# Kernel tuning notes

Measured on AMD Instinct MI355X. Metric: run time of the kernel, lower is better.

## Reference

```python
import jax, jax.numpy as jnp
import numpy as np
from jax import lax

B, T, IN, H, OUT = 4096, 512, 2, 12, 2


def setup_inputs() -> dict:
    key = jax.random.key(0)
    ks = jax.random.split(key, 11)
    s = 1.0 / np.sqrt(H)  # PyTorch LSTM init scale
    f32 = jnp.float32
    return {
        "x": jax.random.normal(ks[0], (B, T, IN), dtype=f32),
        "W_ih0": jax.random.uniform(ks[1], (4 * H, IN), dtype=f32, minval=-s, maxval=s),
        "W_hh0": jax.random.uniform(ks[2], (4 * H, H), dtype=f32, minval=-s, maxval=s),
        "b_ih0": jax.random.uniform(ks[3], (4 * H,), dtype=f32, minval=-s, maxval=s),
        "b_hh0": jax.random.uniform(ks[4], (4 * H,), dtype=f32, minval=-s, maxval=s),
        "W_ih1": jax.random.uniform(ks[5], (4 * H, H), dtype=f32, minval=-s, maxval=s),
        "W_hh1": jax.random.uniform(ks[6], (4 * H, H), dtype=f32, minval=-s, maxval=s),
        "b_ih1": jax.random.uniform(ks[7], (4 * H,), dtype=f32, minval=-s, maxval=s),
        "b_hh1": jax.random.uniform(ks[8], (4 * H,), dtype=f32, minval=-s, maxval=s),
        "fc_W": jax.random.uniform(ks[9], (OUT, H), dtype=f32, minval=-s, maxval=s),
        "fc_b": jax.random.uniform(ks[10], (OUT,), dtype=f32, minval=-s, maxval=s),
    }


def _lstm_layer(x, W_ih, W_hh, b_ih, b_hh):
    # x: [B, T, in_dim] -> hidden trajectory [B, T, H]
    b, h = x.shape[0], W_hh.shape[1]
    # Precompute input contribution for all timesteps: [T, B, 4H]
    xg = jnp.einsum('bti,gi->tbg', x, W_ih) + b_ih + b_hh

    def step(carry, xg_t):
        hprev, cprev = carry
        gates = xg_t + hprev @ W_hh.T  # [B, 4H], PyTorch gate order i,f,g,o
        i, f, g, o = jnp.split(gates, 4, axis=-1)
        i = jax.nn.sigmoid(i)
        f = jax.nn.sigmoid(f)
        g = jnp.tanh(g)
        o = jax.nn.sigmoid(o)
        c = f * cprev + i * g
        hnew = o * jnp.tanh(c)
        return (hnew, c), hnew

    z = jnp.zeros((b, h), dtype=x.dtype)
    _, hs = lax.scan(step, (z, z), xg)  # hs: [T, B, H]
    return jnp.swapaxes(hs, 0, 1)  # [B, T, H]


def reference(x, W_ih0, W_hh0, b_ih0, b_hh0, W_ih1, W_hh1, b_ih1, b_hh1, fc_W, fc_b):
    # 2-layer LSTM, h0=c0=0; dropout is identity in eval mode.
    h1 = _lstm_layer(x, W_ih0, W_hh0, b_ih0, b_hh0)   # [B, T, H]
    h2 = _lstm_layer(h1, W_ih1, W_hh1, b_ih1, b_hh1)  # [B, T, H]
    last = h2[:, -1, :]                               # [B, H]
    return last @ fc_W.T + fc_b                       # [B, OUT]
```

## Files before the change

### kernel.cpp

```cpp
#include <hip/hip_runtime.h>


namespace {
constexpr int H  = 12;
constexpr int T  = 512;
constexpr float LOG2E = 1.4426950408889634f;

typedef float f2 __attribute__((ext_vector_type(2)));
typedef float f4 __attribute__((ext_vector_type(4)));

__device__ __forceinline__ f2 pkfma(f2 a, f2 b, f2 c) {
    asm("v_pk_fma_f32 %0, %1, %2, %0" : "+v"(c) : "v"(a), "v"(b));
    return c;
}
__device__ __forceinline__ f2 pkmul(f2 a, f2 b) {
    f2 d; asm("v_pk_mul_f32 %0, %1, %2" : "=v"(d) : "v"(a), "v"(b)); return d;
}
__device__ __forceinline__ f2 pkadd(f2 a, f2 b) {
    f2 d; asm("v_pk_add_f32 %0, %1, %2" : "=v"(d) : "v"(a), "v"(b)); return d;
}
__device__ __forceinline__ float exp2_(float x) {
    float r; asm("v_exp_f32 %0, %1" : "=v"(r) : "v"(x)); return r;
}
__device__ __forceinline__ float rcp_(float x) { return __builtin_amdgcn_rcpf(x); }
__device__ __forceinline__ void memfence_() { asm volatile("" ::: "memory"); }

template <int CTRL>
__device__ __forceinline__ float dppf(float v) {
    return __int_as_float(__builtin_amdgcn_update_dpp(
        __float_as_int(v), __float_as_int(v), CTRL, 0xF, 0xF, true));
}
constexpr int QP1 = 0x39;
constexpr int QP2 = 0x4E;
constexpr int QP3 = 0x93;
}

__global__ __launch_bounds__(256, 4) void lstm2_fc_kernel(
    const float* __restrict__ x,
    const float* __restrict__ W_ih0,
    const float* __restrict__ W_hh0,
    const float* __restrict__ b_ih0,
    const float* __restrict__ b_hh0,
    const float* __restrict__ W_ih1,
    const float* __restrict__ W_hh1,
    const float* __restrict__ b_ih1,
    const float* __restrict__ b_hh1,
    const float* __restrict__ fc_W,
    const float* __restrict__ fc_b,
    float* __restrict__ out)
{
    const int lane = threadIdx.x & 63;
    const int wid  = __builtin_amdgcn_readfirstlane((int)threadIdx.x >> 6);
    const int b    = blockIdx.x * 4 + wid;
    const int u    = lane >> 2;
    const int gate = lane & 3;
    const int uc   = (u < H) ? u : 0;
    const int r    = gate * H + uc;

    const float pre  = (gate == 2) ? 2.0f : 1.0f;
    const float kmul = -LOG2E * pre;
    const float pa   = 1.0f - pre;
    const float km2  = -2.0f * LOG2E;

    __shared__ __align__(16) float sm[4 * 32];
    float* smb = &sm[wid * 32];
    const bool writer = (gate == 0) && (u < H);
    float* smw0 = smb + uc;
    float* smw1 = smb + 16 + uc;

    f2 wx, whh0p[6], wih1p[6], whh1p[6];
    wx.x = kmul * W_ih0[r * 2 + 0];
    wx.y = kmul * W_ih0[r * 2 + 1];
#pragma unroll
    for (int k = 0; k < 6; ++k) {
        whh0p[k].x = kmul * W_hh0[r * H + 2 * k];
        whh0p[k].y = kmul * W_hh0[r * H + 2 * k + 1];
        wih1p[k].x = kmul * W_ih1[r * H + 2 * k];
        wih1p[k].y = kmul * W_ih1[r * H + 2 * k + 1];
        whh1p[k].x = kmul * W_hh1[r * H + 2 * k];
        whh1p[k].y = kmul * W_hh1[r * H + 2 * k + 1];
    }
    f2 bias0p, bias1p;
    bias0p.x = kmul * (b_ih0[r] + b_hh0[r]); bias0p.y = 0.0f;
    bias1p.x = kmul * (b_ih1[r] + b_hh1[r]); bias1p.y = 0.0f;

    float c0 = 0.0f, c1 = 0.0f;
    f2 hp0[6], hq1[6];
#pragma unroll
    for (int k = 0; k < 6; ++k) { hp0[k] = (f2)(0.0f); hq1[k] = (f2)(0.0f); }

    const f4* xb4 = (const f4*)(x + (size_t)b * T * 2);
    f4 xq = xb4[0];

    auto step = [&](f2 xv) {
        f2 cA = pkfma(wx, xv, bias0p);
        cA = pkfma(whh0p[0], hp0[0], cA);
        cA = pkfma(whh0p[1], hp0[1], cA);
        f2 cB = pkmul(whh0p[2], hp0[2]);
        cB = pkfma(whh0p[3], hp0[3], cB);
        f2 cC = pkmul(whh0p[4], hp0[4]);
        cC = pkfma(whh0p[5], hp0[5], cC);
        cA = pkadd(cA, cB);
        cA = pkadd(cA, cC);
        const float s0 = fmaf(pre, rcp_(1.0f + exp2_(cA.x + cA.y)), pa);
        const float f0v = dppf<QP1>(s0);
        const float g0v = dppf<QP2>(s0);
        const float o0v = dppf<QP3>(s0);
        c0 = fmaf(f0v, c0, s0 * g0v);
        const float h0v = o0v * fmaf(2.0f, rcp_(1.0f + exp2_(km2 * c0)), -1.0f);
        if (writer) *smw0 = h0v;

        f2 dA = pkfma(whh1p[0], hq1[0], bias1p);
        dA = pkfma(whh1p[1], hq1[1], dA);
        f2 dB = pkmul(whh1p[2], hq1[2]);
        dB = pkfma(whh1p[3], hq1[3], dB);
        f2 dC = pkmul(whh1p[4], hq1[4]);
        dC = pkfma(whh1p[5], hq1[5], dC);
        memfence_();
#pragma unroll
        for (int k = 0; k < 6; ++k) {
            hp0[k].x = smb[2 * k];
            hp0[k].y = smb[2 * k + 1];
        }
        dA = pkfma(wih1p[0], hp0[0], dA);
        dA = pkfma(wih1p[1], hp0[1], dA);
        dB = pkfma(wih1p[2], hp0[2], dB);
        dB = pkfma(wih1p[3], hp0[3], dB);
        dC = pkfma(wih1p[4], hp0[4], dC);
        dC = pkfma(wih1p[5], hp0[5], dC);
        dA = pkadd(dA, dB);
        dA = pkadd(dA, dC);
        const float s1 = fmaf(pre, rcp_(1.0f + exp2_(dA.x + dA.y)), pa);
        const float f1v = dppf<QP1>(s1);
        const float g1v = dppf<QP2>(s1);
        const float o1v = dppf<QP3>(s1);
        c1 = fmaf(f1v, c1, s1 * g1v);
        const float h1v = o1v * fmaf(2.0f, rcp_(1.0f + exp2_(km2 * c1)), -1.0f);
        if (writer) *smw1 = h1v;
        memfence_();
#pragma unroll
        for (int k = 0; k < 6; ++k) {
            hq1[k].x = smb[16 + 2 * k];
            hq1[k].y = smb[16 + 2 * k + 1];
        }
    };

    for (int tt = 0; tt < T / 2 - 1; ++tt) {
        const f4 xn = xb4[tt + 1];
        f2 xa; xa.x = xq.x; xa.y = xq.y;
        step(xa);
        f2 xb; xb.x = xq.z; xb.y = xq.w;
        step(xb);
        xq = xn;
    }
    {
        f2 xa; xa.x = xq.x; xa.y = xq.y;
        step(xa);
        f2 xb; xb.x = xq.z; xb.y = xq.w;
        step(xb);
    }

    if (lane == 0) {
        float r0 = fc_b[0];
        float r1 = fc_b[1];
#pragma unroll
        for (int k = 0; k < 6; ++k) {
            r0 = fmaf(fc_W[2 * k],     hq1[k].x, r0);
            r0 = fmaf(fc_W[2 * k + 1], hq1[k].y, r0);
            r1 = fmaf(fc_W[H + 2 * k],     hq1[k].x, r1);
            r1 = fmaf(fc_W[H + 2 * k + 1], hq1[k].y, r1);
        }
        float2 res; res.x = r0; res.y = r1;
        *(float2*)(out + (size_t)b * 2) = res;
    }
}

extern "C" void kernel_launch(void* const* d_in, const int* in_sizes, int n_in,
                              void* d_out, int out_size, void* d_ws, size_t ws_size,
                              hipStream_t stream) {
    const float* x     = (const float*)d_in[0];
    const float* W_ih0 = (const float*)d_in[1];
    const float* W_hh0 = (const float*)d_in[2];
    const float* b_ih0 = (const float*)d_in[3];
    const float* b_hh0 = (const float*)d_in[4];
    const float* W_ih1 = (const float*)d_in[5];
    const float* W_hh1 = (const float*)d_in[6];
    const float* b_ih1 = (const float*)d_in[7];
    const float* b_hh1 = (const float*)d_in[8];
    const float* fc_W  = (const float*)d_in[9];
    const float* fc_b  = (const float*)d_in[10];
    float* out = (float*)d_out;

    lstm2_fc_kernel<<<1024, 256, 0, stream>>>(
        x, W_ih0, W_hh0, b_ih0, b_hh0,
        W_ih1, W_hh1, b_ih1, b_hh1, fc_W, fc_b, out);
}
```

Measured before the change: 279.6 us.

## Merge layer cell updates into one shared-memory exchange per step

Gate lanes now broadcast the activated gates with quad-broadcast DPP. Lane 0 of each quad updates the layer-0 cell and lane 1 updates the layer-1 cell, using layer-1 gates carried over from the previous iteration, so both hidden states are published in one LDS exchange per step instead of two. Layer 1 is skewed one step behind and finished in an epilogue, and the LDS reads are vectorised to f2. This shortens the serial dependency chain per timestep, but it adds selects, and the loop is no longer unrolled by two over x.

```diff
diff --git a/kernel.cpp b/kernel.cpp
--- a/kernel.cpp
+++ b/kernel.cpp
@@ -7,7 +7,6 @@
 constexpr float LOG2E = 1.4426950408889634f;
 
 typedef float f2 __attribute__((ext_vector_type(2)));
-typedef float f4 __attribute__((ext_vector_type(4)));
 
 __device__ __forceinline__ f2 pkfma(f2 a, f2 b, f2 c) {
     asm("v_pk_fma_f32 %0, %1, %2, %0" : "+v"(c) : "v"(a), "v"(b));
@@ -30,9 +29,14 @@
     return __int_as_float(__builtin_amdgcn_update_dpp(
         __float_as_int(v), __float_as_int(v), CTRL, 0xF, 0xF, true));
 }
-constexpr int QP1 = 0x39;
-constexpr int QP2 = 0x4E;
-constexpr int QP3 = 0x93;
+constexpr int BC0 = 0x00;
+constexpr int BC1 = 0x55;
+constexpr int BC2 = 0xAA;
+constexpr int BC3 = 0xFF;
+
+__device__ __forceinline__ float tanh_(float c) {
+    return fmaf(2.0f, rcp_(1.0f + exp2_(-2.0f * LOG2E * c)), -1.0f);
+}
 }
 
 __global__ __launch_bounds__(256, 4) void lstm2_fc_kernel(
@@ -60,13 +64,12 @@
     const float pre  = (gate == 2) ? 2.0f : 1.0f;
     const float kmul = -LOG2E * pre;
     const float pa   = 1.0f - pre;
-    const float km2  = -2.0f * LOG2E;
 
     __shared__ __align__(16) float sm[4 * 32];
     float* smb = &sm[wid * 32];
-    const bool writer = (gate == 0) && (u < H);
-    float* smw0 = smb + uc;
-    float* smw1 = smb + 16 + uc;
+    const bool isL1 = (gate == 1);
+    const bool pub  = (gate <= 1) && (u < H);
+    float* smw = smb + (isL1 ? 16 : 0) + uc;
 
     f2 wx, whh0p[6], wih1p[6], whh1p[6];
     wx.x = kmul * W_ih0[r * 2 + 0];
@@ -84,15 +87,16 @@
     bias0p.x = kmul * (b_ih0[r] + b_hh0[r]); bias0p.y = 0.0f;
     bias1p.x = kmul * (b_ih1[r] + b_hh1[r]); bias1p.y = 0.0f;
 
-    float c0 = 0.0f, c1 = 0.0f;
+    float c = 0.0f;
+    float I1s = 0.0f, F1s = 0.0f, G1s = 0.0f, O1s = 0.0f;
     f2 hp0[6], hq1[6];
 #pragma unroll
     for (int k = 0; k < 6; ++k) { hp0[k] = (f2)(0.0f); hq1[k] = (f2)(0.0f); }
 
-    const f4* xb4 = (const f4*)(x + (size_t)b * T * 2);
-    f4 xq = xb4[0];
+    const float* xp = x + (size_t)b * T * 2;
 
-    auto step = [&](f2 xv) {
+    auto step = [&](float xv0, float xv1) {
+        f2 xv; xv.x = xv0; xv.y = xv1;
         f2 cA = pkfma(wx, xv, bias0p);
         cA = pkfma(whh0p[0], hp0[0], cA);
         cA = pkfma(whh0p[1], hp0[1], cA);
@@ -100,75 +104,67 @@
         cB = pkfma(whh0p[3], hp0[3], cB);
         f2 cC = pkmul(whh0p[4], hp0[4]);
         cC = pkfma(whh0p[5], hp0[5], cC);
-        cA = pkadd(cA, cB);
-        cA = pkadd(cA, cC);
+        cA = pkadd(cA, pkadd(cB, cC));
         const float s0 = fmaf(pre, rcp_(1.0f + exp2_(cA.x + cA.y)), pa);
-        const float f0v = dppf<QP1>(s0);
-        const float g0v = dppf<QP2>(s0);
-        const float o0v = dppf<QP3>(s0);
-        c0 = fmaf(f0v, c0, s0 * g0v);
-        const float h0v = o0v * fmaf(2.0f, rcp_(1.0f + exp2_(km2 * c0)), -1.0f);
-        if (writer) *smw0 = h0v;
-
-        f2 dA = pkfma(whh1p[0], hq1[0], bias1p);
-        dA = pkfma(whh1p[1], hq1[1], dA);
-        f2 dB = pkmul(whh1p[2], hq1[2]);
-        dB = pkfma(whh1p[3], hq1[3], dB);
-        f2 dC = pkmul(whh1p[4], hq1[4]);
-        dC = pkfma(whh1p[5], hq1[5], dC);
+        const float I0 = dppf<BC0>(s0);
+        const float F0 = dppf<BC1>(s0);
+        const float G0 = dppf<BC2>(s0);
+        const float O0 = dppf<BC3>(s0);
+        const float I = isL1 ? I1s : I0;
+        const float F = isL1 ? F1s : F0;
+        const float G = isL1 ? G1s : G0;
+        const float O = isL1 ? O1s : O0;
+        c = fmaf(F, c, I * G);
+        const float hv = O * tanh_(c);
+        if (pub) *smw = hv;
         memfence_();
 #pragma unroll
-        for (int k = 0; k < 6; ++k) {
-            hp0[k].x = smb[2 * k];
-            hp0[k].y = smb[2 * k + 1];
-        }
+        for (int k = 0; k < 6; ++k) hp0[k] = *(const f2*)(smb + 2 * k);
+#pragma unroll
+        for (int k = 0; k < 6; ++k) hq1[k] = *(const f2*)(smb + 16 + 2 * k);
+        f2 dA = pkfma(whh1p[0], hq1[0], bias1p);
         dA = pkfma(wih1p[0], hp0[0], dA);
+        dA = pkfma(whh1p[1], hq1[1], dA);
         dA = pkfma(wih1p[1], hp0[1], dA);
+        f2 dB = pkmul(whh1p[2], hq1[2]);
         dB = pkfma(wih1p[2], hp0[2], dB);
+        dB = pkfma(whh1p[3], hq1[3], dB);
         dB = pkfma(wih1p[3], hp0[3], dB);
+        f2 dC = pkmul(whh1p[4], hq1[4]);
         dC = pkfma(wih1p[4], hp0[4], dC);
+        dC = pkfma(whh1p[5], hq1[5], dC);
         dC = pkfma(wih1p[5], hp0[5], dC);
-        dA = pkadd(dA, dB);
-        dA = pkadd(dA, dC);
+        dA = pkadd(dA, pkadd(dB, dC));
         const float s1 = fmaf(pre, rcp_(1.0f + exp2_(dA.x + dA.y)), pa);
-        const float f1v = dppf<QP1>(s1);
-        const float g1v = dppf<QP2>(s1);
-        const float o1v = dppf<QP3>(s1);
-        c1 = fmaf(f1v, c1, s1 * g1v);
-        const float h1v = o1v * fmaf(2.0f, rcp_(1.0f + exp2_(km2 * c1)), -1.0f);
-        if (writer) *smw1 = h1v;
-        memfence_();
-#pragma unroll
-        for (int k = 0; k < 6; ++k) {
-            hq1[k].x = smb[16 + 2 * k];
-            hq1[k].y = smb[16 + 2 * k + 1];
-        }
+        I1s = dppf<BC0>(s1);
+        F1s = dppf<BC1>(s1);
+        G1s = dppf<BC2>(s1);
+        O1s = dppf<BC3>(s1);
     };
 
-    for (int tt = 0; tt < T / 2 - 1; ++tt) {
-        const f4 xn = xb4[tt + 1];
-        f2 xa; xa.x = xq.x; xa.y = xq.y;
-        step(xa);
-        f2 xb; xb.x = xq.z; xb.y = xq.w;
-        step(xb);
-        xq = xn;
+    float2 xc = *(const float2*)xp;
+    for (int t = 0; t < T - 1; ++t) {
+        const float2 xn = *(const float2*)(xp + 2 * (t + 1));
+        step(xc.x, xc.y);
+        xc = xn;
     }
+    step(xc.x, xc.y);
+
     {
-        f2 xa; xa.x = xq.x; xa.y = xq.y;
-        step(xa);
-        f2 xb; xb.x = xq.z; xb.y = xq.w;
-        step(xb);
+        const float cE = fmaf(F1s, c, I1s * G1s);
+        const float hE = O1s * tanh_(cE);
+        if (pub && isL1) *smw = hE;
+        memfence_();
     }
 
     if (lane == 0) {
         float r0 = fc_b[0];
         float r1 = fc_b[1];
 #pragma unroll
-        for (int k = 0; k < 6; ++k) {
-            r0 = fmaf(fc_W[2 * k],     hq1[k].x, r0);
-            r0 = fmaf(fc_W[2 * k + 1], hq1[k].y, r0);
-            r1 = fmaf(fc_W[H + 2 * k],     hq1[k].x, r1);
-            r1 = fmaf(fc_W[H + 2 * k + 1], hq1[k].y, r1);
+        for (int j = 0; j < H; ++j) {
+            const float hj = smb[16 + j];
+            r0 = fmaf(fc_W[j],     hj, r0);
+            r1 = fmaf(fc_W[H + j], hj, r1);
         }
         float2 res; res.x = r0; res.y = r1;
         *(float2*)(out + (size_t)b * 2) = res;
```

Result: faster. 264.4 us (-5.4%).
